# Kernel tuning notes

Measured on AMD Instinct MI355X. Metric: run time of the kernel, lower is better.

## Reference

```python
import jax, jax.numpy as jnp
import numpy as np

EPS = 1e-10

def _iou(a, b):
    """IoU for boxes in (cx, cy, w, h) format; a, b: (..., 4)."""
    a_min = a[..., :2] - a[..., 2:] * 0.5
    a_max = a[..., :2] + a[..., 2:] * 0.5
    b_min = b[..., :2] - b[..., 2:] * 0.5
    b_max = b[..., :2] + b[..., 2:] * 0.5
    inter_wh = jnp.clip(jnp.minimum(a_max, b_max) - jnp.maximum(a_min, b_min), 0.0)
    inter = inter_wh[..., 0] * inter_wh[..., 1]
    area_a = a[..., 2] * a[..., 3]
    area_b = b[..., 2] * b[..., 3]
    return inter / (area_a + area_b - inter + EPS)

def setup_inputs() -> dict:
    key = jax.random.key(0)
    k1, k2, k3 = jax.random.split(key, 3)
    BATCH, S, C = 16384, 7, 30
    # uniform in (0.01, 1) so sqrt() of w,h channels is finite/differentiable
    preds = jax.random.uniform(k1, (BATCH, S, S, C), jnp.float32, 0.01, 1.0)
    labels = jax.random.uniform(k2, (BATCH, S, S, C), jnp.float32, 0.01, 1.0)
    obj = jax.random.bernoulli(k3, 0.15, (BATCH, S, S)).astype(jnp.float32)
    labels = labels.at[..., 4].set(obj)  # code branches on labels[...,4] == 1
    return {"preds": preds, "labels": labels}

def reference(preds, labels):
    batch = preds.shape[0]
    obj = labels[..., 4] == 1.0  # (B, S, S)
    # faithful quirk: label bbox x-coord is read transposed (labels[i, y, x, 0])
    lb0 = jnp.swapaxes(labels[..., 0], 1, 2)
    lbox = jnp.stack([lb0, labels[..., 1], labels[..., 2], labels[..., 3]], axis=-1)
    iou1 = _iou(preds[..., 0:4], lbox)
    iou2 = _iou(preds[..., 5:9], lbox)
    choose1 = iou1 > iou2
    # branch where box 1 is responsible
    b1 = (5.0 * jnp.sum((preds[..., 0:2] - labels[..., 0:2]) ** 2, -1)
          + jnp.sum((jnp.sqrt(preds[..., 2:4]) - jnp.sqrt(labels[..., 2:4])) ** 2, -1)
          + (iou1 - preds[..., 4]) ** 2
          + 0.5 * preds[..., 9] ** 2)
    # branch where box 2 is responsible (targets read from labels[...,5:9] as in source)
    b2 = (5.0 * jnp.sum((preds[..., 5:7] - labels[..., 5:7]) ** 2, -1)
          + jnp.sum((jnp.sqrt(preds[..., 7:9]) - jnp.sqrt(labels[..., 7:9])) ** 2, -1)
          + (iou2 - preds[..., 9]) ** 2
          + 0.5 * preds[..., 4] ** 2)
    cls = jnp.sum((labels[..., 10:] - preds[..., 10:]) ** 2, -1)
    obj_loss = jnp.where(choose1, b1, b2) + cls
    noobj_loss = 0.5 * (preds[..., 4] ** 2 + preds[..., 9] ** 2)
    total = jnp.sum(jnp.where(obj, obj_loss, noobj_loss))
    return total / batch
```

## Files before the change

### kernel.cpp

```cpp
#include <hip/hip_runtime.h>


#define BATCH 16384
#define S 7
#define C 30
#define NCELLS (BATCH * S * S)
#define BLOCK 256
#define NC 256
#define NBLK (NCELLS / NC)
#define F4_PER_ARR (NC * C / 4)

__device__ __forceinline__ float sq(float v) { return v * v; }

__device__ __forceinline__ float iou_box(float acx, float acy, float aw, float ah,
                                         float bcx, float bcy, float bw, float bh) {
    float ax0 = acx - aw * 0.5f, ax1 = acx + aw * 0.5f;
    float ay0 = acy - ah * 0.5f, ay1 = acy + ah * 0.5f;
    float bx0 = bcx - bw * 0.5f, bx1 = bcx + bw * 0.5f;
    float by0 = bcy - bh * 0.5f, by1 = bcy + bh * 0.5f;
    float iw = fmaxf(fminf(ax1, bx1) - fmaxf(ax0, bx0), 0.0f);
    float ih = fmaxf(fminf(ay1, by1) - fmaxf(ay0, by0), 0.0f);
    float inter = iw * ih;
    float denom = aw * ah + bw * bh - inter + 1e-10f;
    return inter / denom;
}

__global__ __launch_bounds__(BLOCK) void yolo_partial_kernel(
        const float* __restrict__ preds,
        const float* __restrict__ labels,
        float* __restrict__ partials) {
    __shared__ float sp[NC * C];
    __shared__ float sl[NC * C];

    const int tid = threadIdx.x;
    const int base_cell = blockIdx.x * NC;

    const float4* gp = reinterpret_cast<const float4*>(preds  + (size_t)base_cell * C);
    const float4* gl = reinterpret_cast<const float4*>(labels + (size_t)base_cell * C);
    float4* s4p = reinterpret_cast<float4*>(sp);
    float4* s4l = reinterpret_cast<float4*>(sl);
    #pragma unroll
    for (int k = 0; k < 8; ++k) {
        int idx = k * BLOCK + tid;
        if (idx < F4_PER_ARR) {
            s4p[idx] = gp[idx];
            s4l[idx] = gl[idx];
        }
    }
    __syncthreads();

    const float* p = sp + tid * C;
    const float* l = sl + tid * C;
    float pv[C], lv[C];
    #pragma unroll
    for (int i = 0; i < C / 2; ++i) {
        float2 tp = *reinterpret_cast<const float2*>(p + 2 * i);
        pv[2 * i] = tp.x; pv[2 * i + 1] = tp.y;
        float2 tl = *reinterpret_cast<const float2*>(l + 2 * i);
        lv[2 * i] = tl.x; lv[2 * i + 1] = tl.y;
    }

    int cell = base_cell + tid;
    int b    = cell / (S * S);
    int rem  = cell - b * (S * S);
    int y    = rem / S;
    int x    = rem - y * S;
    int pc   = b * (S * S) + x * S + y;
    float lb0;
    if (pc >= base_cell && pc < base_cell + NC) {
        lb0 = sl[(pc - base_cell) * C];
    } else {
        lb0 = labels[(size_t)pc * C];
    }

    float iou1 = iou_box(pv[0], pv[1], pv[2], pv[3], lb0, lv[1], lv[2], lv[3]);
    float iou2 = iou_box(pv[5], pv[6], pv[7], pv[8], lb0, lv[1], lv[2], lv[3]);

    float b1 = 5.0f * (sq(pv[0] - lv[0]) + sq(pv[1] - lv[1]))
             + sq(sqrtf(pv[2]) - sqrtf(lv[2])) + sq(sqrtf(pv[3]) - sqrtf(lv[3]))
             + sq(iou1 - pv[4])
             + 0.5f * pv[9] * pv[9];

    float b2 = 5.0f * (sq(pv[5] - lv[5]) + sq(pv[6] - lv[6]))
             + sq(sqrtf(pv[7]) - sqrtf(lv[7])) + sq(sqrtf(pv[8]) - sqrtf(lv[8]))
             + sq(iou2 - pv[9])
             + 0.5f * pv[4] * pv[4];

    float cls = 0.0f;
    #pragma unroll
    for (int c = 10; c < C; ++c) cls += sq(lv[c] - pv[c]);

    float obj_loss   = ((iou1 > iou2) ? b1 : b2) + cls;
    float noobj_loss = 0.5f * (pv[4] * pv[4] + pv[9] * pv[9]);
    float loss = (lv[4] == 1.0f) ? obj_loss : noobj_loss;

    #pragma unroll
    for (int off = 32; off > 0; off >>= 1)
        loss += __shfl_down(loss, off, 64);

    __shared__ float wsum[BLOCK / 64];
    int lane = tid & 63;
    int wv   = tid >> 6;
    if (lane == 0) wsum[wv] = loss;
    __syncthreads();
    if (tid == 0) {
        partials[blockIdx.x] = wsum[0] + wsum[1] + wsum[2] + wsum[3];
    }
}

__global__ __launch_bounds__(BLOCK) void yolo_reduce_kernel(
        const float* __restrict__ partials,
        float* __restrict__ out) {
    const int tid = threadIdx.x;
    float s = 0.0f;
    for (int i = tid; i < NBLK; i += BLOCK) s += partials[i];

    #pragma unroll
    for (int off = 32; off > 0; off >>= 1)
        s += __shfl_down(s, off, 64);

    __shared__ float wsum[BLOCK / 64];
    int lane = tid & 63;
    int wv   = tid >> 6;
    if (lane == 0) wsum[wv] = s;
    __syncthreads();
    if (tid == 0) {
        out[0] = (wsum[0] + wsum[1] + wsum[2] + wsum[3]) * (1.0f / (float)BATCH);
    }
}

extern "C" void kernel_launch(void* const* d_in, const int* in_sizes, int n_in,
                              void* d_out, int out_size, void* d_ws, size_t ws_size,
                              hipStream_t stream) {
    const float* preds  = (const float*)d_in[0];
    const float* labels = (const float*)d_in[1];
    float* out = (float*)d_out;
    float* partials = (float*)d_ws;

    yolo_partial_kernel<<<NBLK, BLOCK, 0, stream>>>(preds, labels, partials);
    yolo_reduce_kernel<<<1, BLOCK, 0, stream>>>(partials, out);
}
```

Baseline: 208.9 us.

## Load cell data directly from global memory into registers, dropping LDS staging

Removes the shared-memory staging of 256 cells of preds and labels, along with its __syncthreads. Each thread now reads its own 30 floats straight from global memory as float2 loads and always reads the transposed lb0 value from global. Launch bounds now request 2 blocks per SM. The intent is to remove the 60KB-per-block LDS footprint that limits occupancy, plus the barrier and LDS traffic. The cost is strided, uncoalesced per-thread loads (120-byte stride between lanes), which rely on the cache to merge accesses.

```diff
diff --git a/kernel.cpp b/kernel.cpp
--- a/kernel.cpp
+++ b/kernel.cpp
@@ -6,9 +6,7 @@
 #define C 30
 #define NCELLS (BATCH * S * S)
 #define BLOCK 256
-#define NC 256
-#define NBLK (NCELLS / NC)
-#define F4_PER_ARR (NC * C / 4)
+#define NBLK (NCELLS / BLOCK)
 
 __device__ __forceinline__ float sq(float v) { return v * v; }
 
@@ -25,52 +23,34 @@
     return inter / denom;
 }
 
-__global__ __launch_bounds__(BLOCK) void yolo_partial_kernel(
+__global__ __launch_bounds__(BLOCK, 2) void yolo_partial_kernel(
         const float* __restrict__ preds,
         const float* __restrict__ labels,
         float* __restrict__ partials) {
-    __shared__ float sp[NC * C];
-    __shared__ float sl[NC * C];
+    const int tid  = threadIdx.x;
+    const int cell = blockIdx.x * BLOCK + tid;
 
-    const int tid = threadIdx.x;
-    const int base_cell = blockIdx.x * NC;
-
-    const float4* gp = reinterpret_cast<const float4*>(preds  + (size_t)base_cell * C);
-    const float4* gl = reinterpret_cast<const float4*>(labels + (size_t)base_cell * C);
-    float4* s4p = reinterpret_cast<float4*>(sp);
-    float4* s4l = reinterpret_cast<float4*>(sl);
-    #pragma unroll
-    for (int k = 0; k < 8; ++k) {
-        int idx = k * BLOCK + tid;
-        if (idx < F4_PER_ARR) {
-            s4p[idx] = gp[idx];
-            s4l[idx] = gl[idx];
-        }
-    }
-    __syncthreads();
-
-    const float* p = sp + tid * C;
-    const float* l = sl + tid * C;
-    float pv[C], lv[C];
-    #pragma unroll
-    for (int i = 0; i < C / 2; ++i) {
-        float2 tp = *reinterpret_cast<const float2*>(p + 2 * i);
-        pv[2 * i] = tp.x; pv[2 * i + 1] = tp.y;
-        float2 tl = *reinterpret_cast<const float2*>(l + 2 * i);
-        lv[2 * i] = tl.x; lv[2 * i + 1] = tl.y;
-    }
-
-    int cell = base_cell + tid;
     int b    = cell / (S * S);
     int rem  = cell - b * (S * S);
     int y    = rem / S;
     int x    = rem - y * S;
     int pc   = b * (S * S) + x * S + y;
-    float lb0;
-    if (pc >= base_cell && pc < base_cell + NC) {
-        lb0 = sl[(pc - base_cell) * C];
-    } else {
-        lb0 = labels[(size_t)pc * C];
+
+    const float2* pG = reinterpret_cast<const float2*>(preds  + (size_t)cell * C);
+    const float2* lG = reinterpret_cast<const float2*>(labels + (size_t)cell * C);
+
+    float2 tp[15], tl[15];
+    #pragma unroll
+    for (int i = 0; i < 15; ++i) tp[i] = pG[i];
+    #pragma unroll
+    for (int i = 0; i < 15; ++i) tl[i] = lG[i];
+    float lb0 = labels[(size_t)pc * C];
+
+    float pv[C], lv[C];
+    #pragma unroll
+    for (int i = 0; i < 15; ++i) {
+        pv[2 * i] = tp[i].x; pv[2 * i + 1] = tp[i].y;
+        lv[2 * i] = tl[i].x; lv[2 * i + 1] = tl[i].y;
     }
 
     float iou1 = iou_box(pv[0], pv[1], pv[2], pv[3], lb0, lv[1], lv[2], lv[3]);
```

Result: slower. 218.3 us (+4.5%).
